# Performance work log

Hardware: AMD Instinct MI355X
Metric: run time of the kernel (lower is better)

The kernel has to match this reference:

```python
import jax, jax.numpy as jnp
import numpy as np


def setup_inputs() -> dict:
    key = jax.random.key(0)
    ks = jax.random.split(key, 16)
    N, E, G = 50000, 800000, 50
    in_dim, hidden, K, pdim, L, n_classes = 128, 128, 3, 2, 4, 10
    npg = N // G  # nodes per graph
    eg = jax.random.randint(ks[0], (E,), 0, G)
    src = eg * npg + jax.random.randint(ks[1], (E,), 0, npg)
    dst = eg * npg + jax.random.randint(ks[2], (E,), 0, npg)
    graph_ids = jnp.arange(N, dtype=jnp.int32) // npg
    f = lambda k, s, sc: jax.random.normal(k, s, dtype=jnp.float32) * sc
    return {
        'x': f(ks[3], (N, in_dim), 1.0),
        'emb_W': f(ks[4], (in_dim, hidden), 0.05),
        'emb_b': jnp.zeros((hidden,), jnp.float32),
        'fc_W': f(ks[5], (L, hidden, K * hidden), 0.05),
        'fc_b': jnp.zeros((L, K * hidden), jnp.float32),
        'mu': f(ks[6], (L, K, pdim), 0.1),
        'inv_sigma': jnp.ones((L, K, pdim), jnp.float32) + f(ks[7], (L, K, pdim), 0.01),
        'bn_gamma': jnp.ones((L, hidden), jnp.float32),
        'bn_beta': jnp.zeros((L, hidden), jnp.float32),
        'pp_W': f(ks[8], (L, 2, pdim), 0.5),
        'pp_b': jnp.zeros((L, pdim), jnp.float32),
        'mlp_W1': f(ks[9], (hidden, hidden // 2), 0.1),
        'mlp_b1': jnp.zeros((hidden // 2,), jnp.float32),
        'mlp_W2': f(ks[10], (hidden // 2, hidden // 4), 0.1),
        'mlp_b2': jnp.zeros((hidden // 4,), jnp.float32),
        'mlp_W3': f(ks[11], (hidden // 4, n_classes), 0.1),
        'mlp_b3': jnp.zeros((n_classes,), jnp.float32),
        'src': src, 'dst': dst, 'graph_ids': graph_ids, 'n_graphs': G,
    }


def reference(x, emb_W, emb_b, fc_W, fc_b, mu, inv_sigma, bn_gamma, bn_beta,
              pp_W, pp_b, mlp_W1, mlp_b1, mlp_W2, mlp_b2, mlp_W3, mlp_b3,
              src, dst, graph_ids, n_graphs):
    N = x.shape[0]
    L, K, pdim = mu.shape
    eps = 1e-5
    # node embedding
    h = x @ emb_W + emb_b  # [N, H]
    # in-degrees and edge pseudo coordinates (compute_pseudo)
    deg = jax.ops.segment_sum(jnp.ones(dst.shape, x.dtype), dst, num_segments=N)
    pseudo = jnp.stack([jax.lax.rsqrt(deg[src] + 1.0), jax.lax.rsqrt(deg[dst] + 1.0)], axis=-1)  # [E, 2]
    for i in range(L):
        h_in = h
        out_dim = fc_W.shape[2] // K
        # pseudo projection: Linear(2, dim) + tanh
        p = jnp.tanh(pseudo @ pp_W[i] + pp_b[i])  # [E, pdim]
        # node projection into K kernels
        hp = (h @ fc_W[i] + fc_b[i]).reshape(N, K, out_dim)  # [N, K, O]
        # Gaussian kernel weights per edge
        diff = p[:, None, :] - mu[i][None, :, :]             # [E, K, pdim]
        gw = jnp.exp(-0.5 * jnp.sum((diff * inv_sigma[i][None]) ** 2, axis=-1))  # [E, K]
        # message = sum_k w_ek * hp[src, k, :]; then sum-aggregate at dst
        m = jnp.einsum('ek,eko->eo', gw, hp[src])            # [E, O]
        h = jax.ops.segment_sum(m, dst, num_segments=N)      # [N, O]
        # batch norm (training-mode batch statistics over nodes)
        mean = jnp.mean(h, axis=0)
        var = jnp.var(h, axis=0)
        h = (h - mean) * jax.lax.rsqrt(var + eps) * bn_gamma[i] + bn_beta[i]
        h = jax.nn.relu(h)
        h = h_in + h  # residual (in_dim == out_dim for all layers)
    # mean readout per graph
    counts = jax.ops.segment_sum(jnp.ones((N,), h.dtype), graph_ids, num_segments=n_graphs)
    hg = jax.ops.segment_sum(h, graph_ids, num_segments=n_graphs) / counts[:, None]
    # MLPReadout: two halving ReLU layers + output layer
    y = jax.nn.relu(hg @ mlp_W1 + mlp_b1)
    y = jax.nn.relu(y @ mlp_W2 + mlp_b2)
    return y @ mlp_W3 + mlp_b3
```

## Files before the change

### kernel.cpp

```cpp
#include <hip/hip_runtime.h>


typedef unsigned char  u8;
typedef unsigned short u16;
typedef unsigned int   u32;
typedef __attribute__((ext_vector_type(8))) short bf16x8;
typedef __attribute__((ext_vector_type(4))) float f32x4;

__device__ __forceinline__ u16 f2b(float f) {
    union { float f; u32 u; } v; v.f = f;
    u32 u = v.u;
    u32 r = (u + 0x7fffu + ((u >> 16) & 1u)) >> 16;
    return (u16)r;
}
__device__ __forceinline__ float blo(u32 h) {
    union { u32 u; float f; } v; v.u = h << 16; return v.f;
}
__device__ __forceinline__ float bhi(u32 h) {
    union { u32 u; float f; } v; v.u = h & 0xffff0000u; return v.f;
}

__global__ void prep_weights(const float* __restrict__ embW, u16* __restrict__ embT,
                             const float* __restrict__ fcW, u16* __restrict__ fcT,
                             int totalFc) {
    int idx = blockIdx.x * 256 + threadIdx.x;
    if (idx < 16384) {
        int n = idx >> 7, k = idx & 127;
        embT[idx] = f2b(embW[k * 128 + n]);
        return;
    }
    idx -= 16384;
    if (idx >= totalFc) return;
    int kk = idx % 384;
    int rest = idx / 384;
    int n = rest & 127;
    int l = rest >> 7;
    int kc = kk >> 7, r = kk & 127;
    fcT[idx] = f2b(fcW[((size_t)(l * 128 + r)) * 384 + kc * 128 + n]);
}

__global__ void hist_kernel(const int* __restrict__ dst, int* __restrict__ cnt, int E) {
    int e = blockIdx.x * 256 + threadIdx.x;
    if (e < E) atomicAdd(&cnt[dst[e]], 1);
}

__global__ void scan_partial(const int* __restrict__ cnt, int* __restrict__ bsum, int N) {
    __shared__ int buf[256];
    int t = threadIdx.x, base = blockIdx.x * 256;
    buf[t] = (base + t < N) ? cnt[base + t] : 0;
    __syncthreads();
    for (int off = 128; off > 0; off >>= 1) {
        if (t < off) buf[t] += buf[t + off];
        __syncthreads();
    }
    if (t == 0) bsum[blockIdx.x] = buf[0];
}
__global__ void scan_bsums(const int* __restrict__ bsum, int* __restrict__ boff, int nb) {
    __shared__ int buf[256];
    int t = threadIdx.x;
    int v = (t < nb) ? bsum[t] : 0;
    buf[t] = v;
    __syncthreads();
    for (int off = 1; off < 256; off <<= 1) {
        int x = (t >= off) ? buf[t - off] : 0;
        __syncthreads();
        buf[t] += x;
        __syncthreads();
    }
    if (t < nb) boff[t] = buf[t] - v;
}
__global__ void scan_final(const int* __restrict__ cnt, const int* __restrict__ boff,
                           int* __restrict__ rs, int N) {
    __shared__ int buf[256];
    int t = threadIdx.x, base = blockIdx.x * 256;
    int v = (base + t < N) ? cnt[base + t] : 0;
    buf[t] = v;
    __syncthreads();
    for (int off = 1; off < 256; off <<= 1) {
        int x = (t >= off) ? buf[t - off] : 0;
        __syncthreads();
        buf[t] += x;
        __syncthreads();
    }
    if (base + t < N) rs[base + t + 1] = boff[blockIdx.x] + buf[t];
    if (base == 0 && t == 0) rs[0] = 0;
}

__global__ __launch_bounds__(256) void bucketA(const int* __restrict__ src,
                                               const int* __restrict__ dst,
                                               const int* __restrict__ rs,
                                               int* __restrict__ gcur,
                                               u32* __restrict__ tmp,
                                               int E, int npg, int G) {
    __shared__ u32 ebuf[4096];
    __shared__ u8  gmap[4096];
    __shared__ int ghist[64], gexc[64], gbase[64], lcur[64];
    const int tid = threadIdx.x;
    const int e0 = blockIdx.x * 4096;
    const int n = min(4096, E - e0);
    if (tid < 64) { ghist[tid] = 0; lcur[tid] = 0; }
    __syncthreads();
    for (int i = tid; i < n; i += 256) {
        int g = dst[e0 + i] / npg;
        atomicAdd(&ghist[g], 1);
    }
    __syncthreads();
    if (tid == 0) {
        int acc = 0;
        for (int g = 0; g < G; g++) { gexc[g] = acc; acc += ghist[g]; }
    }
    __syncthreads();
    if (tid < G) {
        int c = ghist[tid];
        gbase[tid] = (c > 0) ? rs[tid * npg] + atomicAdd(&gcur[tid], c) : 0;
    }
    __syncthreads();
    for (int i = tid; i < n; i += 256) {
        int d = dst[e0 + i];
        int g = d / npg;
        int pos = gexc[g] + atomicAdd(&lcur[g], 1);
        ebuf[pos] = ((u32)src[e0 + i] << 16) | (u32)(d - g * npg);
        gmap[pos] = (u8)g;
    }
    __syncthreads();
    for (int i = tid; i < n; i += 256) {
        int g = gmap[i];
        tmp[gbase[g] + (i - gexc[g])] = ebuf[i];
    }
}

__global__ __launch_bounds__(1024) void bucketB(const u32* __restrict__ tmp,
                                                const int* __restrict__ rs,
                                                int* __restrict__ psrc,
                                                int* __restrict__ pdst,
                                                int npg) {
    __shared__ int rsl[1025];
    __shared__ int lcur[1024];
    const int g = blockIdx.x, tid = threadIdx.x;
    const int base = g * npg;
    for (int i = tid; i <= npg; i += 1024) rsl[i] = rs[base + i];
    for (int i = tid; i < npg; i += 1024) lcur[i] = 0;
    __syncthreads();
    const int p0 = rsl[0], p1 = rsl[npg];
    for (int p = p0 + tid; p < p1; p += 1024) {
        u32 v = tmp[p];
        int dl = v & 0xffffu;
        int pos = rsl[dl] + atomicAdd(&lcur[dl], 1);
        psrc[pos] = (int)(v >> 16);
    }
    for (int i = tid; i < npg; i += 1024) {
        int a = rsl[i], b = rsl[i + 1];
        for (int p = a; p < b; p++) pdst[p] = base + i;
    }
}

__global__ void gw_kernel(const int* __restrict__ psrc, const int* __restrict__ pdst,
                          const int* __restrict__ cnt,
                          const float* __restrict__ ppW, const float* __restrict__ ppb,
                          const float* __restrict__ mu, const float* __restrict__ isig,
                          uint2* __restrict__ rec, int E, int Epad, int L) {
    int p = blockIdx.x * 256 + threadIdx.x;
    if (p >= Epad) return;
    if (p >= E) {
        for (int l = 0; l < L; l++) rec[(size_t)l * Epad + p] = make_uint2(0u, 0u);
        return;
    }
    int s = psrc[p];
    float ps0 = rsqrtf((float)cnt[s] + 1.0f);
    float ps1 = rsqrtf((float)cnt[pdst[p]] + 1.0f);
    for (int l = 0; l < L; l++) {
        float p0 = tanhf(ps0 * ppW[l * 4 + 0] + ps1 * ppW[l * 4 + 2] + ppb[l * 2 + 0]);
        float p1 = tanhf(ps0 * ppW[l * 4 + 1] + ps1 * ppW[l * 4 + 3] + ppb[l * 2 + 1]);
        float g[3];
#pragma unroll
        for (int k = 0; k < 3; k++) {
            float d0 = (p0 - mu[(l * 3 + k) * 2 + 0]) * isig[(l * 3 + k) * 2 + 0];
            float d1 = (p1 - mu[(l * 3 + k) * 2 + 1]) * isig[(l * 3 + k) * 2 + 1];
            g[k] = expf(-0.5f * (d0 * d0 + d1 * d1));
        }
        uint2 r;
        r.x = (u32)s | ((u32)f2b(g[0]) << 16);
        r.y = (u32)f2b(g[1]) | ((u32)f2b(g[2]) << 16);
        rec[(size_t)l * Epad + p] = r;
    }
}

__global__ __launch_bounds__(256) void agg_kernel(const u16* __restrict__ hb,
                                                  const uint2* __restrict__ rec,
                                                  const int* __restrict__ rs,
                                                  u16* __restrict__ t,
                                                  float* __restrict__ sk, int N) {
    int nid = blockIdx.x * 16 + (threadIdx.x >> 4);
    if (nid >= N) return;
    int lane = threadIdx.x & 15;
    int p0 = rs[nid], p1 = rs[nid + 1];
    float a0[8] = {}, a1[8] = {}, a2[8] = {};
    float gs0 = 0.f, gs1 = 0.f, gs2 = 0.f;
    int p = p0;
    for (; p + 4 <= p1; p += 4) {
        uint2 rv[4];
        uint4 hv[4];
#pragma unroll
        for (int j = 0; j < 4; j++) rv[j] = rec[p + j];
#pragma unroll
        for (int j = 0; j < 4; j++) {
            int s = rv[j].x & 0xffff;
            hv[j] = *(const uint4*)(hb + (size_t)s * 128 + lane * 8);
        }
#pragma unroll
        for (int j = 0; j < 4; j++) {
            float g0 = bhi(rv[j].x), g1 = blo(rv[j].y), g2 = bhi(rv[j].y);
            float f[8];
            f[0] = blo(hv[j].x); f[1] = bhi(hv[j].x);
            f[2] = blo(hv[j].y); f[3] = bhi(hv[j].y);
            f[4] = blo(hv[j].z); f[5] = bhi(hv[j].z);
            f[6] = blo(hv[j].w); f[7] = bhi(hv[j].w);
#pragma unroll
            for (int c = 0; c < 8; c++) {
                a0[c] += g0 * f[c];
                a1[c] += g1 * f[c];
                a2[c] += g2 * f[c];
            }
            gs0 += g0; gs1 += g1; gs2 += g2;
        }
    }
    if (p < p1) {
        uint2 rv[4];
        uint4 hv[4];
#pragma unroll
        for (int j = 0; j < 4; j++) rv[j] = rec[p + j];
#pragma unroll
        for (int j = 0; j < 4; j++) {
            int s = rv[j].x & 0xffff;
            hv[j] = *(const uint4*)(hb + (size_t)s * 128 + lane * 8);
        }
#pragma unroll
        for (int j = 0; j < 4; j++) {
            bool ok = (p + j) < p1;
            float g0 = ok ? bhi(rv[j].x) : 0.f;
            float g1 = ok ? blo(rv[j].y) : 0.f;
            float g2 = ok ? bhi(rv[j].y) : 0.f;
            float f[8];
            f[0] = blo(hv[j].x); f[1] = bhi(hv[j].x);
            f[2] = blo(hv[j].y); f[3] = bhi(hv[j].y);
            f[4] = blo(hv[j].z); f[5] = bhi(hv[j].z);
            f[6] = blo(hv[j].w); f[7] = bhi(hv[j].w);
#pragma unroll
            for (int c = 0; c < 8; c++) {
                a0[c] += g0 * f[c];
                a1[c] += g1 * f[c];
                a2[c] += g2 * f[c];
            }
            gs0 += g0; gs1 += g1; gs2 += g2;
        }
    }
    size_t base = (size_t)nid * 384 + lane * 8;
    uint4 o;
    o.x = (u32)f2b(a0[0]) | ((u32)f2b(a0[1]) << 16);
    o.y = (u32)f2b(a0[2]) | ((u32)f2b(a0[3]) << 16);
    o.z = (u32)f2b(a0[4]) | ((u32)f2b(a0[5]) << 16);
    o.w = (u32)f2b(a0[6]) | ((u32)f2b(a0[7]) << 16);
    *(uint4*)(t + base) = o;
    o.x = (u32)f2b(a1[0]) | ((u32)f2b(a1[1]) << 16);
    o.y = (u32)f2b(a1[2]) | ((u32)f2b(a1[3]) << 16);
    o.z = (u32)f2b(a1[4]) | ((u32)f2b(a1[5]) << 16);
    o.w = (u32)f2b(a1[6]) | ((u32)f2b(a1[7]) << 16);
    *(uint4*)(t + base + 128) = o;
    o.x = (u32)f2b(a2[0]) | ((u32)f2b(a2[1]) << 16);
    o.y = (u32)f2b(a2[2]) | ((u32)f2b(a2[3]) << 16);
    o.z = (u32)f2b(a2[4]) | ((u32)f2b(a2[5]) << 16);
    o.w = (u32)f2b(a2[6]) | ((u32)f2b(a2[7]) << 16);
    *(uint4*)(t + base + 256) = o;
    if (lane == 0) {
        sk[nid * 4 + 0] = gs0;
        sk[nid * 4 + 1] = gs1;
        sk[nid * 4 + 2] = gs2;
        sk[nid * 4 + 3] = 0.f;
    }
}

__global__ __launch_bounds__(256) void gemm_mfma(const void* __restrict__ Araw,
                                                 const u16* __restrict__ Bt,
                                                 int M, int KD,
                                                 const float* __restrict__ bias,
                                                 const float* __restrict__ sk,
                                                 u16* __restrict__ outB,
                                                 int mode,
                                                 float* __restrict__ bnred) {
    __shared__ u16 As[128 * 64];
    __shared__ u16 Bs[128 * 64];
    const int m0 = blockIdx.x * 128;
    const int tid = threadIdx.x;
    const int lane = tid & 63;
    const int w = tid >> 6;
    const int wr = w >> 1, wc = w & 1;

    f32x4 acc[4][4];
#pragma unroll
    for (int m = 0; m < 4; m++)
#pragma unroll
        for (int n = 0; n < 4; n++) acc[m][n] = (f32x4){0.f, 0.f, 0.f, 0.f};

    for (int k0 = 0; k0 < KD; k0 += 64) {
        __syncthreads();
        if (mode == 0) {
            const float* Af = (const float*)Araw;
#pragma unroll
            for (int i = 0; i < 4; i++) {
                int idx = tid + i * 256;
                int r = idx >> 3, g = idx & 7;
                int gs = g ^ (r & 7);
                uint4 av = make_uint4(0, 0, 0, 0);
                if (m0 + r < M) {
                    float4 v0 = *(const float4*)(Af + (size_t)(m0 + r) * KD + k0 + g * 8);
                    float4 v1 = *(const float4*)(Af + (size_t)(m0 + r) * KD + k0 + g * 8 + 4);
                    av.x = (u32)f2b(v0.x) | ((u32)f2b(v0.y) << 16);
                    av.y = (u32)f2b(v0.z) | ((u32)f2b(v0.w) << 16);
                    av.z = (u32)f2b(v1.x) | ((u32)f2b(v1.y) << 16);
                    av.w = (u32)f2b(v1.z) | ((u32)f2b(v1.w) << 16);
                }
                *(uint4*)(As + r * 64 + gs * 8) = av;
                uint4 bv = *(const uint4*)(Bt + (size_t)r * KD + k0 + g * 8);
                *(uint4*)(Bs + r * 64 + gs * 8) = bv;
            }
        } else {
            const u16* Ab = (const u16*)Araw;
#pragma unroll
            for (int i = 0; i < 4; i++) {
                int blk = w * 4 + i;
                int r = blk * 8 + (lane >> 3);
                int gsrc = (lane & 7) ^ (r & 7);
                const u16* gA = Ab + (size_t)(m0 + r) * KD + k0 + gsrc * 8;
                const u16* gB = Bt + (size_t)r * KD + k0 + gsrc * 8;
                __builtin_amdgcn_global_load_lds(
                    (const __attribute__((address_space(1))) void*)gA,
                    (__attribute__((address_space(3))) void*)(As + blk * 512 + lane * 8),
                    16, 0, 0);
                __builtin_amdgcn_global_load_lds(
                    (const __attribute__((address_space(1))) void*)gB,
                    (__attribute__((address_space(3))) void*)(Bs + blk * 512 + lane * 8),
                    16, 0, 0);
            }
        }
        __syncthreads();
#pragma unroll
        for (int kk = 0; kk < 2; kk++) {
            bf16x8 af[4], bfr[4];
#pragma unroll
            for (int m = 0; m < 4; m++) {
                int r = wr * 64 + m * 16 + (lane & 15);
                int g = (kk * 4 + (lane >> 4)) ^ (r & 7);
                af[m] = *(const bf16x8*)(As + r * 64 + g * 8);
            }
#pragma unroll
            for (int n = 0; n < 4; n++) {
                int r = wc * 64 + n * 16 + (lane & 15);
                int g = (kk * 4 + (lane >> 4)) ^ (r & 7);
                bfr[n] = *(const bf16x8*)(Bs + r * 64 + g * 8);
            }
#pragma unroll
            for (int m = 0; m < 4; m++)
#pragma unroll
                for (int n = 0; n < 4; n++)
                    acc[m][n] = __builtin_amdgcn_mfma_f32_16x16x32_bf16(af[m], bfr[n], acc[m][n], 0, 0, 0);
        }
    }

    if (mode == 0) {
#pragma unroll
        for (int n = 0; n < 4; n++) {
            int col = wc * 64 + n * 16 + (lane & 15);
            float bv = bias[col];
#pragma unroll
            for (int m = 0; m < 4; m++) {
#pragma unroll
                for (int j = 0; j < 4; j++) {
                    int row = m0 + wr * 64 + m * 16 + (lane >> 4) * 4 + j;
                    if (row < M) outB[(size_t)row * 128 + col] = f2b(acc[m][n][j] + bv);
                }
            }
        }
    } else {
        float colsum[4] = {0.f, 0.f, 0.f, 0.f};
        float colsq[4]  = {0.f, 0.f, 0.f, 0.f};
#pragma unroll
        for (int n = 0; n < 4; n++) {
            int col = wc * 64 + n * 16 + (lane & 15);
            float b0 = bias[col], b1 = bias[128 + col], b2 = bias[256 + col];
#pragma unroll
            for (int m = 0; m < 4; m++) {
#pragma unroll
                for (int j = 0; j < 4; j++) {
                    int row = m0 + wr * 64 + m * 16 + (lane >> 4) * 4 + j;
                    if (row < M) {
                        float4 skv = *(const float4*)(sk + row * 4);
                        float v = acc[m][n][j] + skv.x * b0 + skv.y * b1 + skv.z * b2;
                        outB[(size_t)row * 128 + col] = f2b(v);
                        colsum[n] += v;
                        colsq[n]  += v * v;
                    }
                }
            }
        }
        __syncthreads();
        float* red = (float*)As;
        if (tid < 256) red[tid] = 0.f;
        __syncthreads();
#pragma unroll
        for (int n = 0; n < 4; n++) {
            float s = colsum[n], q = colsq[n];
            s += __shfl_xor(s, 16); s += __shfl_xor(s, 32);
            q += __shfl_xor(q, 16); q += __shfl_xor(q, 32);
            if (lane < 16) {
                int col = wc * 64 + n * 16 + lane;
                atomicAdd(&red[col], s);
                atomicAdd(&red[128 + col], q);
            }
        }
        __syncthreads();
        if (tid < 256) atomicAdd(&bnred[tid], red[tid]);
    }
}

__global__ void bn_apply(u16* __restrict__ hb,
                         const u16* __restrict__ aggB,
                         const float* __restrict__ bnred,
                         const float* __restrict__ gamma, const float* __restrict__ beta,
                         float invN, int N) {
    int idx = blockIdx.x * 256 + threadIdx.x;
    if (idx >= N * 32) return;
    int c4 = idx & 31;
    float4 s  = *(const float4*)(bnred + c4 * 4);
    float4 q  = *(const float4*)(bnred + 128 + c4 * 4);
    float4 ga = *(const float4*)(gamma + c4 * 4);
    float4 be = *(const float4*)(beta + c4 * 4);
    float4 sc, sh;
    {
        float m, v2;
        m = s.x * invN; v2 = q.x * invN - m * m; sc.x = ga.x * rsqrtf(v2 + 1e-5f); sh.x = be.x - m * sc.x;
        m = s.y * invN; v2 = q.y * invN - m * m; sc.y = ga.y * rsqrtf(v2 + 1e-5f); sh.y = be.y - m * sc.y;
        m = s.z * invN; v2 = q.z * invN - m * m; sc.z = ga.z * rsqrtf(v2 + 1e-5f); sh.z = be.z - m * sc.z;
        m = s.w * invN; v2 = q.w * invN - m * m; sc.w = ga.w * rsqrtf(v2 + 1e-5f); sh.w = be.w - m * sc.w;
    }
    uint2 av = ((const uint2*)aggB)[idx];
    uint2 hv = ((const uint2*)hb)[idx];
    float r0 = blo(hv.x) + fmaxf(blo(av.x) * sc.x + sh.x, 0.f);
    float r1 = bhi(hv.x) + fmaxf(bhi(av.x) * sc.y + sh.y, 0.f);
    float r2 = blo(hv.y) + fmaxf(blo(av.y) * sc.z + sh.z, 0.f);
    float r3 = bhi(hv.y) + fmaxf(bhi(av.y) * sc.w + sh.w, 0.f);
    uint2 o;
    o.x = (u32)f2b(r0) | ((u32)f2b(r1) << 16);
    o.y = (u32)f2b(r2) | ((u32)f2b(r3) << 16);
    ((uint2*)hb)[idx] = o;
}

__global__ void readout_kernel(const u16* __restrict__ hb, const int* __restrict__ gids,
                               float* __restrict__ hg, float* __restrict__ cnts, int N) {
    int c = threadIdx.x;
    int r0 = blockIdx.x * 25;
    if (r0 >= N) return;
    int r1 = min(r0 + 25, N);
    int cur = gids[r0];
    float acc = 0.f, cnt = 0.f;
    for (int r = r0; r < r1; r++) {
        int g = gids[r];
        if (g != cur) {
            atomicAdd(&hg[(size_t)cur * 128 + c], acc);
            if (c == 0) atomicAdd(&cnts[cur], cnt);
            acc = 0.f; cnt = 0.f; cur = g;
        }
        acc += blo((u32)hb[(size_t)r * 128 + c]);
        cnt += 1.f;
    }
    atomicAdd(&hg[(size_t)cur * 128 + c], acc);
    if (c == 0) atomicAdd(&cnts[cur], cnt);
}

__global__ void mlp_kernel(const float* __restrict__ hg, const float* __restrict__ cnts,
                           const float* __restrict__ W1, const float* __restrict__ b1,
                           const float* __restrict__ W2, const float* __restrict__ b2,
                           const float* __restrict__ W3, const float* __restrict__ b3,
                           float* __restrict__ out) {
    __shared__ float v[128], y1[64], y2[32];
    int g = blockIdx.x, t = threadIdx.x;
    float inv = 1.0f / cnts[g];
    v[t] = hg[(size_t)g * 128 + t] * inv;
    __syncthreads();
    if (t < 64) {
        float a = b1[t];
        for (int k = 0; k < 128; k++) a += v[k] * W1[k * 64 + t];
        y1[t] = fmaxf(a, 0.f);
    }
    __syncthreads();
    if (t < 32) {
        float a = b2[t];
        for (int k = 0; k < 64; k++) a += y1[k] * W2[k * 32 + t];
        y2[t] = fmaxf(a, 0.f);
    }
    __syncthreads();
    if (t < 10) {
        float a = b3[t];
        for (int k = 0; k < 32; k++) a += y2[k] * W3[k * 10 + t];
        out[g * 10 + t] = a;
    }
}

extern "C" void kernel_launch(void* const* d_in, const int* in_sizes, int n_in,
                              void* d_out, int out_size, void* d_ws, size_t ws_size,
                              hipStream_t stream) {
    const float* x      = (const float*)d_in[0];
    const float* emb_W  = (const float*)d_in[1];
    const float* emb_b  = (const float*)d_in[2];
    const float* fc_W   = (const float*)d_in[3];
    const float* fc_b   = (const float*)d_in[4];
    const float* mu     = (const float*)d_in[5];
    const float* isig   = (const float*)d_in[6];
    const float* gamma  = (const float*)d_in[7];
    const float* beta   = (const float*)d_in[8];
    const float* ppW    = (const float*)d_in[9];
    const float* ppb    = (const float*)d_in[10];
    const float* W1     = (const float*)d_in[11];
    const float* b1     = (const float*)d_in[12];
    const float* W2     = (const float*)d_in[13];
    const float* b2     = (const float*)d_in[14];
    const float* W3     = (const float*)d_in[15];
    const float* b3     = (const float*)d_in[16];
    const int*   src    = (const int*)d_in[17];
    const int*   dst    = (const int*)d_in[18];
    const int*   gids   = (const int*)d_in[19];

    const int N = in_sizes[0] / 128;
    const int E = in_sizes[17];
    const int L = in_sizes[8] / 128;
    const int G = out_size / 10;
    const int npg = N / G;
    const int Epad = E + 16;
    float* out = (float*)d_out;

    char* wp = (char*)d_ws;
    auto alloc = [&](size_t bytes) {
        char* p = wp;
        wp += (bytes + 255) & ~(size_t)255;
        return (void*)p;
    };
    u16*   hb     = (u16*)alloc((size_t)N * 128 * 2);
    u16*   t      = (u16*)alloc((size_t)N * 384 * 2);
    u16*   aggB   = (u16*)alloc((size_t)N * 128 * 2);
    uint2* rec    = (uint2*)alloc((size_t)L * Epad * 8);
    int*   psrc   = (int*)alloc((size_t)E * 4);
    int*   pdst   = (int*)alloc((size_t)E * 4);
    u32*   tmp    = (u32*)alloc((size_t)E * 4);
    float* sk     = (float*)alloc((size_t)N * 4 * 4);
    int*   rs     = (int*)alloc((size_t)(N + 1) * 4);
    int*   bsum   = (int*)alloc(256 * 4);
    int*   boff   = (int*)alloc(256 * 4);
    u16*   wembt  = (u16*)alloc((size_t)128 * 128 * 2);
    u16*   wfct   = (u16*)alloc((size_t)L * 128 * 384 * 2);
    char*  z0     = wp;
    int*   cnt    = (int*)alloc((size_t)N * 4);
    int*   gcur   = (int*)alloc(256 * 4);
    float* hg     = (float*)alloc((size_t)G * 128 * 4);
    float* cnts   = (float*)alloc((size_t)G * 4);
    float* bnAll  = (float*)alloc((size_t)L * 256 * 4);
    size_t zbytes = (size_t)(wp - z0);

    hipMemsetAsync(z0, 0, zbytes, stream);

    const int totalFc = L * 128 * 384;
    prep_weights<<<(16384 + totalFc + 255) / 256, 256, 0, stream>>>(emb_W, wembt, fc_W, wfct, totalFc);

    const int nb = (N + 255) / 256;
    hist_kernel<<<(E + 255) / 256, 256, 0, stream>>>(dst, cnt, E);
    scan_partial<<<nb, 256, 0, stream>>>(cnt, bsum, N);
    scan_bsums<<<1, 256, 0, stream>>>(bsum, boff, nb);
    scan_final<<<nb, 256, 0, stream>>>(cnt, boff, rs, N);
    bucketA<<<(E + 4095) / 4096, 256, 0, stream>>>(src, dst, rs, gcur, tmp, E, npg, G);
    bucketB<<<G, 1024, 0, stream>>>(tmp, rs, psrc, pdst, npg);
    gw_kernel<<<(Epad + 255) / 256, 256, 0, stream>>>(psrc, pdst, cnt, ppW, ppb, mu, isig,
                                                      rec, E, Epad, L);

    const int gblocks = (N + 127) / 128;
    gemm_mfma<<<gblocks, 256, 0, stream>>>(x, wembt, N, 128, emb_b, nullptr, hb, 0, nullptr);

    const float invN = 1.0f / (float)N;
    for (int l = 0; l < L; l++) {
        agg_kernel<<<(N + 15) / 16, 256, 0, stream>>>(hb, rec + (size_t)l * Epad, rs, t, sk, N);
        gemm_mfma<<<gblocks, 256, 0, stream>>>(t, wfct + (size_t)l * 128 * 384, N, 384,
                                               fc_b + (size_t)l * 384, sk, aggB, 1,
                                               bnAll + (size_t)l * 256);
        bn_apply<<<(N * 32 + 255) / 256, 256, 0, stream>>>(hb, aggB, bnAll + (size_t)l * 256,
                                                           gamma + l * 128, beta + l * 128, invN, N);
    }

    readout_kernel<<<(N + 24) / 25, 128, 0, stream>>>(hb, gids, hg, cnts, N);
    mlp_kernel<<<G, 128, 0, stream>>>(hg, cnts, W1, b1, W2, b2, W3, b3, out);
}
```

Before: 424.4 us.

## Build CSR per graph in bucket kernel and fuse final batchnorm into readout

Replaces the global per-node degree histogram and three-pass prefix scan with a per-graph edge histogram and scan. Per-node counts and offsets are now computed inside the per-graph bucketB block, and degrees are derived from row-pointer differences. The last layer's batchnorm/relu/residual is folded into the readout kernel, which skips one full read/write of the node features. This relies on nodes-per-graph fitting in one 1024-thread block.

```diff
diff --git a/kernel.cpp b/kernel.cpp
--- a/kernel.cpp
+++ b/kernel.cpp
@@ -39,56 +39,31 @@
     fcT[idx] = f2b(fcW[((size_t)(l * 128 + r)) * 384 + kc * 128 + n]);
 }
 
-__global__ void hist_kernel(const int* __restrict__ dst, int* __restrict__ cnt, int E) {
-    int e = blockIdx.x * 256 + threadIdx.x;
-    if (e < E) atomicAdd(&cnt[dst[e]], 1);
-}
-
-__global__ void scan_partial(const int* __restrict__ cnt, int* __restrict__ bsum, int N) {
-    __shared__ int buf[256];
-    int t = threadIdx.x, base = blockIdx.x * 256;
-    buf[t] = (base + t < N) ? cnt[base + t] : 0;
-    __syncthreads();
-    for (int off = 128; off > 0; off >>= 1) {
-        if (t < off) buf[t] += buf[t + off];
-        __syncthreads();
-    }
-    if (t == 0) bsum[blockIdx.x] = buf[0];
-}
-__global__ void scan_bsums(const int* __restrict__ bsum, int* __restrict__ boff, int nb) {
-    __shared__ int buf[256];
-    int t = threadIdx.x;
-    int v = (t < nb) ? bsum[t] : 0;
-    buf[t] = v;
-    __syncthreads();
-    for (int off = 1; off < 256; off <<= 1) {
-        int x = (t >= off) ? buf[t - off] : 0;
-        __syncthreads();
-        buf[t] += x;
-        __syncthreads();
-    }
-    if (t < nb) boff[t] = buf[t] - v;
-}
-__global__ void scan_final(const int* __restrict__ cnt, const int* __restrict__ boff,
-                           int* __restrict__ rs, int N) {
-    __shared__ int buf[256];
-    int t = threadIdx.x, base = blockIdx.x * 256;
-    int v = (base + t < N) ? cnt[base + t] : 0;
-    buf[t] = v;
-    __syncthreads();
-    for (int off = 1; off < 256; off <<= 1) {
-        int x = (t >= off) ? buf[t - off] : 0;
-        __syncthreads();
-        buf[t] += x;
-        __syncthreads();
-    }
-    if (base + t < N) rs[base + t + 1] = boff[blockIdx.x] + buf[t];
-    if (base == 0 && t == 0) rs[0] = 0;
+__global__ __launch_bounds__(256) void ghist_kernel(const int* __restrict__ dst,
+                                                    int* __restrict__ gtot,
+                                                    int E, int npg) {
+    __shared__ int h[64];
+    const int tid = threadIdx.x;
+    if (tid < 64) h[tid] = 0;
+    __syncthreads();
+    int e0 = blockIdx.x * 4096;
+    int n = min(4096, E - e0);
+    for (int i = tid; i < n; i += 256) atomicAdd(&h[dst[e0 + i] / npg], 1);
+    __syncthreads();
+    if (tid < 64) { int v = h[tid]; if (v) atomicAdd(&gtot[tid], v); }
+}
+
+__global__ void gscan_kernel(const int* __restrict__ gtot, int* __restrict__ gbase0, int G) {
+    if (threadIdx.x == 0 && blockIdx.x == 0) {
+        int acc = 0;
+        for (int g = 0; g < G; g++) { gbase0[g] = acc; acc += gtot[g]; }
+        gbase0[G] = acc;
+    }
 }
 
 __global__ __launch_bounds__(256) void bucketA(const int* __restrict__ src,
                                                const int* __restrict__ dst,
-                                               const int* __restrict__ rs,
+                                               const int* __restrict__ gbase0,
                                                int* __restrict__ gcur,
                                                u32* __restrict__ tmp,
                                                int E, int npg, int G) {
@@ -112,7 +87,7 @@
     __syncthreads();
     if (tid < G) {
         int c = ghist[tid];
-        gbase[tid] = (c > 0) ? rs[tid * npg] + atomicAdd(&gcur[tid], c) : 0;
+        gbase[tid] = (c > 0) ? gbase0[tid] + atomicAdd(&gcur[tid], c) : 0;
     }
     __syncthreads();
     for (int i = tid; i < n; i += 256) {
@@ -130,23 +105,42 @@
 }
 
 __global__ __launch_bounds__(1024) void bucketB(const u32* __restrict__ tmp,
-                                                const int* __restrict__ rs,
+                                                const int* __restrict__ gbase0,
+                                                int* __restrict__ rs,
                                                 int* __restrict__ psrc,
                                                 int* __restrict__ pdst,
-                                                int npg) {
+                                                int npg, int G, int N) {
     __shared__ int rsl[1025];
     __shared__ int lcur[1024];
+    __shared__ int buf[1024];
     const int g = blockIdx.x, tid = threadIdx.x;
     const int base = g * npg;
-    for (int i = tid; i <= npg; i += 1024) rsl[i] = rs[base + i];
-    for (int i = tid; i < npg; i += 1024) lcur[i] = 0;
-    __syncthreads();
-    const int p0 = rsl[0], p1 = rsl[npg];
-    for (int p = p0 + tid; p < p1; p += 1024) {
-        u32 v = tmp[p];
-        int dl = v & 0xffffu;
+    const int r0 = gbase0[g], r1 = gbase0[g + 1];
+    if (tid < 1024) lcur[tid] = 0;
+    __syncthreads();
+    for (int p = r0 + tid; p < r1; p += 1024)
+        atomicAdd(&lcur[tmp[p] & 0xffffu], 1);
+    __syncthreads();
+    int v = (tid < npg) ? lcur[tid] : 0;
+    buf[tid] = v;
+    __syncthreads();
+    for (int off = 1; off < 1024; off <<= 1) {
+        int x = (tid >= off) ? buf[tid - off] : 0;
+        __syncthreads();
+        buf[tid] += x;
+        __syncthreads();
+    }
+    if (tid < npg) rsl[tid] = r0 + buf[tid] - v;
+    if (tid == 0) rsl[npg] = r1;
+    if (tid < 1024) lcur[tid] = 0;
+    __syncthreads();
+    for (int i = tid; i < npg; i += 1024) rs[base + i] = rsl[i];
+    if (g == G - 1 && tid == 0) rs[N] = r1;
+    for (int p = r0 + tid; p < r1; p += 1024) {
+        u32 w = tmp[p];
+        int dl = w & 0xffffu;
         int pos = rsl[dl] + atomicAdd(&lcur[dl], 1);
-        psrc[pos] = (int)(v >> 16);
+        psrc[pos] = (int)(w >> 16);
     }
     for (int i = tid; i < npg; i += 1024) {
         int a = rsl[i], b = rsl[i + 1];
@@ -155,7 +149,7 @@
 }
 
 __global__ void gw_kernel(const int* __restrict__ psrc, const int* __restrict__ pdst,
-                          const int* __restrict__ cnt,
+                          const int* __restrict__ rs,
                           const float* __restrict__ ppW, const float* __restrict__ ppb,
                           const float* __restrict__ mu, const float* __restrict__ isig,
                           uint2* __restrict__ rec, int E, int Epad, int L) {
@@ -166,8 +160,9 @@
         return;
     }
     int s = psrc[p];
-    float ps0 = rsqrtf((float)cnt[s] + 1.0f);
-    float ps1 = rsqrtf((float)cnt[pdst[p]] + 1.0f);
+    int d = pdst[p];
+    float ps0 = rsqrtf((float)(rs[s + 1] - rs[s]) + 1.0f);
+    float ps1 = rsqrtf((float)(rs[d + 1] - rs[d]) + 1.0f);
     for (int l = 0; l < L; l++) {
         float p0 = tanhf(ps0 * ppW[l * 4 + 0] + ps1 * ppW[l * 4 + 2] + ppb[l * 2 + 0]);
         float p1 = tanhf(ps0 * ppW[l * 4 + 1] + ps1 * ppW[l * 4 + 3] + ppb[l * 2 + 1]);
@@ -454,9 +449,20 @@
     ((uint2*)hb)[idx] = o;
 }
 
-__global__ void readout_kernel(const u16* __restrict__ hb, const int* __restrict__ gids,
-                               float* __restrict__ hg, float* __restrict__ cnts, int N) {
+__global__ void readout_bn_kernel(const u16* __restrict__ hb,
+                                  const u16* __restrict__ aggB,
+                                  const float* __restrict__ bnred,
+                                  const float* __restrict__ gamma,
+                                  const float* __restrict__ beta,
+                                  float invN,
+                                  const int* __restrict__ gids,
+                                  float* __restrict__ hg, float* __restrict__ cnts, int N) {
     int c = threadIdx.x;
+    float s = bnred[c], q = bnred[128 + c];
+    float mean = s * invN;
+    float var  = q * invN - mean * mean;
+    float sc = gamma[c] * rsqrtf(var + 1e-5f);
+    float sh = beta[c] - mean * sc;
     int r0 = blockIdx.x * 25;
     if (r0 >= N) return;
     int r1 = min(r0 + 25, N);
@@ -469,7 +475,9 @@
             if (c == 0) atomicAdd(&cnts[cur], cnt);
             acc = 0.f; cnt = 0.f; cur = g;
         }
-        acc += blo((u32)hb[(size_t)r * 128 + c]);
+        float hval = blo((u32)hb[(size_t)r * 128 + c]);
+        float aval = blo((u32)aggB[(size_t)r * 128 + c]);
+        acc += hval + fmaxf(aval * sc + sh, 0.f);
         cnt += 1.f;
     }
     atomicAdd(&hg[(size_t)cur * 128 + c], acc);
@@ -552,12 +560,11 @@
     u32*   tmp    = (u32*)alloc((size_t)E * 4);
     float* sk     = (float*)alloc((size_t)N * 4 * 4);
     int*   rs     = (int*)alloc((size_t)(N + 1) * 4);
-    int*   bsum   = (int*)alloc(256 * 4);
-    int*   boff   = (int*)alloc(256 * 4);
+    int*   gbase0 = (int*)alloc(256 * 4);
     u16*   wembt  = (u16*)alloc((size_t)128 * 128 * 2);
     u16*   wfct   = (u16*)alloc((size_t)L * 128 * 384 * 2);
     char*  z0     = wp;
-    int*   cnt    = (int*)alloc((size_t)N * 4);
+    int*   gtot   = (int*)alloc(256 * 4);
     int*   gcur   = (int*)alloc(256 * 4);
     float* hg     = (float*)alloc((size_t)G * 128 * 4);
     float* cnts   = (float*)alloc((size_t)G * 4);
@@ -569,14 +576,11 @@
     const int totalFc = L * 128 * 384;
     prep_weights<<<(16384 + totalFc + 255) / 256, 256, 0, stream>>>(emb_W, wembt, fc_W, wfct, totalFc);
 
-    const int nb = (N + 255) / 256;
-    hist_kernel<<<(E + 255) / 256, 256, 0, stream>>>(dst, cnt, E);
-    scan_partial<<<nb, 256, 0, stream>>>(cnt, bsum, N);
-    scan_bsums<<<1, 256, 0, stream>>>(bsum, boff, nb);
-    scan_final<<<nb, 256, 0, stream>>>(cnt, boff, rs, N);
-    bucketA<<<(E + 4095) / 4096, 256, 0, stream>>>(src, dst, rs, gcur, tmp, E, npg, G);
-    bucketB<<<G, 1024, 0, stream>>>(tmp, rs, psrc, pdst, npg);
-    gw_kernel<<<(Epad + 255) / 256, 256, 0, stream>>>(psrc, pdst, cnt, ppW, ppb, mu, isig,
+    ghist_kernel<<<(E + 4095) / 4096, 256, 0, stream>>>(dst, gtot, E, npg);
+    gscan_kernel<<<1, 64, 0, stream>>>(gtot, gbase0, G);
+    bucketA<<<(E + 4095) / 4096, 256, 0, stream>>>(src, dst, gbase0, gcur, tmp, E, npg, G);
+    bucketB<<<G, 1024, 0, stream>>>(tmp, gbase0, rs, psrc, pdst, npg, G, N);
+    gw_kernel<<<(Epad + 255) / 256, 256, 0, stream>>>(psrc, pdst, rs, ppW, ppb, mu, isig,
                                                       rec, E, Epad, L);
 
     const int gblocks = (N + 127) / 128;
@@ -588,10 +592,14 @@
         gemm_mfma<<<gblocks, 256, 0, stream>>>(t, wfct + (size_t)l * 128 * 384, N, 384,
                                                fc_b + (size_t)l * 384, sk, aggB, 1,
                                                bnAll + (size_t)l * 256);
-        bn_apply<<<(N * 32 + 255) / 256, 256, 0, stream>>>(hb, aggB, bnAll + (size_t)l * 256,
-                                                           gamma + l * 128, beta + l * 128, invN, N);
-    }
-
-    readout_kernel<<<(N + 24) / 25, 128, 0, stream>>>(hb, gids, hg, cnts, N);
+        if (l < L - 1)
+            bn_apply<<<(N * 32 + 255) / 256, 256, 0, stream>>>(hb, aggB, bnAll + (size_t)l * 256,
+                                                               gamma + l * 128, beta + l * 128,
+                                                               invN, N);
+    }
+
+    readout_bn_kernel<<<(N + 24) / 25, 128, 0, stream>>>(hb, aggB, bnAll + (size_t)(L - 1) * 256,
+                                                         gamma + (L - 1) * 128, beta + (L - 1) * 128,
+                                                         invN, gids, hg, cnts, N);
     mlp_kernel<<<G, 128, 0, stream>>>(hg, cnts, W1, b1, W2, b2, W3, b3, out);
 }
```

Result: faster. 388.4 us (-8.5%).
